# Kernel optimization log

Measured on AMD Instinct MI355X. Metric: run time of the kernel, lower is better.

## Reference

```python
import jax, jax.numpy as jnp
import numpy as np

D_MODEL = 1024
NUM_HEADS = 16
HEAD_DIM = D_MODEL // NUM_HEADS
MAX_SEQ_LEN = 1024
BATCH = 2
SEQ = 1024


def setup_inputs() -> dict:
    key = jax.random.key(0)
    ks = jax.random.split(key, 12)
    s = 1.0 / np.sqrt(D_MODEL)
    inp = {
        "q": jax.random.normal(ks[0], (BATCH, SEQ, D_MODEL), jnp.float32),
        "k": jax.random.normal(ks[1], (BATCH, SEQ, D_MODEL), jnp.float32),
        "v": jax.random.normal(ks[2], (BATCH, SEQ, D_MODEL), jnp.float32),
        # causal mask (broadcast over batch and heads); masked_fill where mask==0
        "mask": jnp.tril(jnp.ones((SEQ, SEQ), jnp.bool_))[None, None, :, :],
        "Wq": jax.random.normal(ks[3], (D_MODEL, D_MODEL), jnp.float32) * s,
        "bq": jnp.zeros((D_MODEL,), jnp.float32),
        "Wk": jax.random.normal(ks[4], (D_MODEL, D_MODEL), jnp.float32) * s,
        "bk": jnp.zeros((D_MODEL,), jnp.float32),
        "Wv": jax.random.normal(ks[5], (D_MODEL, D_MODEL), jnp.float32) * s,
        "bv": jnp.zeros((D_MODEL,), jnp.float32),
        "Wo": jax.random.normal(ks[6], (D_MODEL, D_MODEL), jnp.float32) * s,
        "bo": jnp.zeros((D_MODEL,), jnp.float32),
        # relative-position embedding table (requires_grad=False in original)
        "e_r": jax.random.normal(ks[7], (MAX_SEQ_LEN, HEAD_DIM), jnp.float32),
    }
    return inp


def _skew(qe):
    # qe: (b, h, q, L) -> pad last dim on the left, reshape, drop first row
    b, h, q, L = qe.shape
    s = jnp.pad(qe, ((0, 0), (0, 0), (0, 0), (1, 0)))  # (b,h,q,L+1)
    s = s.reshape(b, h, L + 1, q)
    return s[:, :, 1:, :]  # (b,h,L,q)


def _rel_position_mask(q_len, L, dtype):
    # keep qe[i, j] where j >= L - 1 - i (upper-right skewed triangle)
    rows = jnp.arange(q_len)
    cols = jnp.arange(L)
    return (cols[None, :] >= (L - 1 - rows)[:, None]).astype(dtype)


def reference(q, k, v, mask, Wq, bq, Wk, bk, Wv, bv, Wo, bo, e_r):
    B, S, _ = q.shape
    def split_heads(x):
        return x.reshape(B, -1, NUM_HEADS, HEAD_DIM).transpose(0, 2, 1, 3)

    qh = split_heads(q @ Wq + bq)  # (B,H,S,D)
    kh = split_heads(k @ Wk + bk)
    vh = split_heads(v @ Wv + bv)

    q_len = qh.shape[2]
    e_sub = e_r[max(0, MAX_SEQ_LEN - q_len):, :]  # (L, D), L = min(q_len, MAX)
    qe = jnp.einsum('bhqd,kd->bhqk', qh, e_sub)  # (B,H,q,L)
    pm = _rel_position_mask(q_len, e_sub.shape[0], qe.dtype)
    qe = qe * pm[None, None, :, :]
    S_rel = _skew(qe)  # (B,H,L,q) == (B,H,S,S)

    scores = jnp.einsum('bhqd,bhkd->bhqk', qh, kh) / np.sqrt(HEAD_DIM)
    if mask is not None:
        scores = jnp.where(mask, scores, -1e9)
    attn = jax.nn.softmax(scores + S_rel, axis=-1)
    out = jnp.einsum('bhqk,bhkd->bhqd', attn, vh)
    out = out.transpose(0, 2, 1, 3).reshape(B, -1, D_MODEL)
    out = out @ Wo + bo
    return out, S_rel, qe
```

## Files before the change

kernel.cpp:

```cpp
#include <hip/hip_runtime.h>
#include <hip/hip_bf16.h>

typedef unsigned short u16;
typedef __attribute__((ext_vector_type(8))) short    bf16x8;
typedef __attribute__((ext_vector_type(8))) unsigned short u16x8;
typedef __attribute__((ext_vector_type(4))) float    f32x4;

#define SEQ    1024
#define DMODEL 1024
#define NHEAD  16
#define HDIM   64

#define OUT_OFF_SREL 2097152UL
#define OUT_OFF_QE   35651584UL

#define MFMA16(a, b, c) __builtin_amdgcn_mfma_f32_16x16x32_bf16((a), (b), (c), 0, 0, 0)

__device__ __forceinline__ float b2f(u16 u) {
    union { unsigned int i; float f; } x; x.i = ((unsigned int)u) << 16; return x.f;
}
__device__ __forceinline__ u16 f2b(float f) {
    union { __hip_bfloat16 h; u16 u; } x; x.h = __float2bfloat16(f); return x.u;
}
__device__ __forceinline__ void st_out(void* p, size_t idx, float v, int isf32) {
    if (isf32) ((float*)p)[idx] = v;
    else       ((u16*)p)[idx]   = f2b(v);
}

__global__ __launch_bounds__(256)
void k_detect(const u16* __restrict__ q, unsigned* __restrict__ flag)
{
    __shared__ int cnt;
    if (threadIdx.x == 0) cnt = 0;
    __syncthreads();
    int plaus = 0;
    for (int i = threadIdx.x; i < 4096; i += 256) {
        u16 u = q[2 * i];
        int e = (u >> 7) & 0xFF;
        if (e >= 102 && e <= 130) plaus++;
    }
    atomicAdd(&cnt, plaus);
    __syncthreads();
    if (threadIdx.x == 0) *flag = (cnt < 2048) ? 1u : 0u;
}

__global__ __launch_bounds__(256)
void k_conv3(const void* __restrict__ s0, const void* __restrict__ s1, const void* __restrict__ s2,
             u16* __restrict__ d0, u16* __restrict__ d1, u16* __restrict__ d2,
             int n4, const unsigned* __restrict__ flag)
{
    const int z = blockIdx.z;
    const void* src = (z == 0) ? s0 : (z == 1) ? s1 : s2;
    u16* dst = (z == 0) ? d0 : (z == 1) ? d1 : d2;
    int i = blockIdx.x * 256 + threadIdx.x;
    if (i >= n4) return;
    if (*flag) {
        float4 f = ((const float4*)src)[i];
        ushort4 o;
        o.x = f2b(f.x); o.y = f2b(f.y); o.z = f2b(f.z); o.w = f2b(f.w);
        ((ushort4*)dst)[i] = o;
    } else {
        ((ushort4*)dst)[i] = ((const ushort4*)src)[i];
    }
}

__global__ __launch_bounds__(256)
void k_conv_small(const void* __restrict__ b0, const void* __restrict__ b1,
                  const void* __restrict__ b2, const void* __restrict__ b3,
                  const void* __restrict__ erp,
                  u16* __restrict__ db0, u16* __restrict__ db1,
                  u16* __restrict__ db2, u16* __restrict__ db3,
                  u16* __restrict__ der, const unsigned* __restrict__ flag)
{
    const int bx = blockIdx.x;
    const void* src; u16* dst; int i;
    if (bx < 64) { src = erp; dst = der; i = bx * 256 + threadIdx.x; }
    else {
        const int which = bx - 64;
        src = (which == 0) ? b0 : (which == 1) ? b1 : (which == 2) ? b2 : b3;
        dst = (which == 0) ? db0 : (which == 1) ? db1 : (which == 2) ? db2 : db3;
        i = threadIdx.x;
    }
    if (*flag) {
        float4 f = ((const float4*)src)[i];
        ushort4 o;
        o.x = f2b(f.x); o.y = f2b(f.y); o.z = f2b(f.z); o.w = f2b(f.w);
        ((ushort4*)dst)[i] = o;
    } else {
        ((ushort4*)dst)[i] = ((const ushort4*)src)[i];
    }
}

__global__ __launch_bounds__(256)
void k_convT4(const void* __restrict__ s0, const void* __restrict__ s1,
              const void* __restrict__ s2, const void* __restrict__ s3,
              u16* __restrict__ d0, u16* __restrict__ d1,
              u16* __restrict__ d2, u16* __restrict__ d3,
              const unsigned* __restrict__ flag)
{
    __shared__ u16 tile[64][65];
    const int z = blockIdx.z;
    const void* src = (z == 0) ? s0 : (z == 1) ? s1 : (z == 2) ? s2 : s3;
    u16* dst = (z == 0) ? d0 : (z == 1) ? d1 : (z == 2) ? d2 : d3;

    const int t  = threadIdx.x;
    const int n0 = blockIdx.x * 64;
    const int k0 = blockIdx.y * 64;
    const int isf32 = (*flag != 0u);

    #pragma unroll
    for (int i = 0; i < 4; ++i) {
        int idx = i * 256 + t;
        int r  = idx >> 4;
        int cg = (idx & 15) << 2;
        if (isf32) {
            float4 f = *(const float4*)((const float*)src + (size_t)(k0 + r) * 1024 + n0 + cg);
            tile[cg + 0][r] = f2b(f.x); tile[cg + 1][r] = f2b(f.y);
            tile[cg + 2][r] = f2b(f.z); tile[cg + 3][r] = f2b(f.w);
        } else {
            ushort4 u = *(const ushort4*)((const u16*)src + (size_t)(k0 + r) * 1024 + n0 + cg);
            tile[cg + 0][r] = u.x; tile[cg + 1][r] = u.y;
            tile[cg + 2][r] = u.z; tile[cg + 3][r] = u.w;
        }
    }
    __syncthreads();
    #pragma unroll
    for (int i = 0; i < 4; ++i) {
        int idx = i * 256 + t;
        int nl = idx >> 4;
        int kg = (idx & 15) << 2;
        ushort4 o;
        o.x = tile[nl][kg + 0]; o.y = tile[nl][kg + 1];
        o.z = tile[nl][kg + 2]; o.w = tile[nl][kg + 3];
        *(ushort4*)(dst + (size_t)(n0 + nl) * 1024 + k0 + kg) = o;
    }
}

__global__ __launch_bounds__(256)
void k_gemm(const u16* __restrict__ Aq, const u16* __restrict__ Ak, const u16* __restrict__ Av,
            const u16* __restrict__ Wtq, const u16* __restrict__ Wtk, const u16* __restrict__ Wtv,
            const u16* __restrict__ Bq, const u16* __restrict__ Bk, const u16* __restrict__ Bv,
            u16* __restrict__ Oq, u16* __restrict__ Ok, u16* __restrict__ Ov,
            void* __restrict__ out_flat, const unsigned* __restrict__ flag, int mode)
{
    __shared__ __align__(16) u16 Xs[128][72];
    __shared__ __align__(16) u16 Ws[128][72];

    const int z = blockIdx.z;
    const u16* A  = (z == 0) ? Aq : (z == 1) ? Ak : Av;
    const u16* Wt = (z == 0) ? Wtq : (z == 1) ? Wtk : Wtv;
    const u16* Bi = (z == 0) ? Bq : (z == 1) ? Bk : Bv;
    u16* O = (z == 0) ? Oq : (z == 1) ? Ok : Ov;

    const int t    = threadIdx.x;
    const int lane = t & 63;
    const int w    = t >> 6;
    const int q4   = lane >> 4;
    const int l16  = lane & 15;
    const int wy   = w >> 1, wx = w & 1;
    const int m0   = blockIdx.y * 128;
    const int n0   = blockIdx.x * 128;

    f32x4 acc[4][4] = {};

    for (int k0 = 0; k0 < DMODEL; k0 += 64) {
        __syncthreads();
        #pragma unroll
        for (int i = 0; i < 4; ++i) {
            int idx = i * 256 + t;
            int row = idx >> 3;
            int kg  = (idx & 7) << 3;
            *(u16x8*)&Xs[row][kg] = *(const u16x8*)(A  + (size_t)(m0 + row) * 1024 + k0 + kg);
            *(u16x8*)&Ws[row][kg] = *(const u16x8*)(Wt + (size_t)(n0 + row) * 1024 + k0 + kg);
        }
        __syncthreads();
        #pragma unroll
        for (int kc = 0; kc < 2; ++kc) {
            bf16x8 af[4], bfr[4];
            #pragma unroll
            for (int mt = 0; mt < 4; ++mt)
                af[mt] = *(const bf16x8*)&Xs[wy * 64 + mt * 16 + l16][kc * 32 + q4 * 8];
            #pragma unroll
            for (int nt = 0; nt < 4; ++nt)
                bfr[nt] = *(const bf16x8*)&Ws[wx * 64 + nt * 16 + l16][kc * 32 + q4 * 8];
            #pragma unroll
            for (int mt = 0; mt < 4; ++mt)
                #pragma unroll
                for (int nt = 0; nt < 4; ++nt)
                    acc[mt][nt] = MFMA16(af[mt], bfr[nt], acc[mt][nt]);
        }
    }

    const int isf32 = (*flag != 0u);
    float bias[4];
    #pragma unroll
    for (int nt = 0; nt < 4; ++nt) bias[nt] = b2f(Bi[n0 + wx * 64 + nt * 16 + l16]);

    #pragma unroll
    for (int mt = 0; mt < 4; ++mt) {
        #pragma unroll
        for (int nt = 0; nt < 4; ++nt) {
            #pragma unroll
            for (int reg = 0; reg < 4; ++reg) {
                const int m = m0 + wy * 64 + mt * 16 + q4 * 4 + reg;
                const int n = n0 + wx * 64 + nt * 16 + l16;
                const float v = acc[mt][nt][reg] + bias[nt];
                if (mode == 0) {
                    const int b = m >> 10, s = m & 1023, h = n >> 6, d = n & 63;
                    O[(((size_t)(b * NHEAD + h)) * SEQ + s) * HDIM + d] = f2b(v);
                } else {
                    st_out(out_flat, (size_t)m * DMODEL + n, v, isf32);
                }
            }
        }
    }
}

__global__ __launch_bounds__(256)
void k_attn(const u16* __restrict__ qh, const u16* __restrict__ kh, const u16* __restrict__ vh,
            const u16* __restrict__ er, u16* __restrict__ opre,
            void* __restrict__ out, const unsigned* __restrict__ flag)
{
    __shared__ __align__(16) u16 Ks[64][72];
    __shared__ __align__(16) u16 Vt[64][72];
    __shared__ __align__(16) u16 Es[128][72];
    __shared__ float Rs[4][16][130];
    __shared__ __align__(16) u16 Ps[4][16][72];

    const int t    = threadIdx.x;
    const int lane = t & 63;
    const int w    = t >> 6;
    const int q4   = lane >> 4;
    const int l16  = lane & 15;
    const int bh   = blockIdx.x;
    const int qt   = 15 - blockIdx.y;
    const int r0   = qt * 64;
    const int isf32 = (*flag != 0u);
    const size_t obase = (size_t)bh * (SEQ * SEQ);

    for (int ml = w; ml < 64; ml += 4) {
        const int r  = r0 + ml;
        const int Lz = SEQ - 1 - r;
        const size_t rq = OUT_OFF_QE   + obase + (size_t)r * SEQ;
        const size_t rs = OUT_OFF_SREL + obase + (size_t)r * SEQ + r + 1;
        for (int c2 = lane; c2 < Lz; c2 += 64) {
            st_out(out, rq + c2, 0.f, isf32);
            st_out(out, rs + c2, 0.f, isf32);
        }
    }

    bf16x8 aQ[2];
    #pragma unroll
    for (int kc = 0; kc < 2; ++kc)
        aQ[kc] = *(const bf16x8*)(qh + ((size_t)bh * SEQ + r0 + w * 16 + l16) * HDIM + kc * 32 + q4 * 8);

    f32x4 Oacc[4] = {};
    float mi[4] = { -1e30f, -1e30f, -1e30f, -1e30f };
    float li[4] = {};

    for (int tt = 0; tt <= qt; ++tt) {
        const int c0 = tt * 64;
        const int jbase = 960 + c0 - r0;
        const int diag = (tt == qt);

        __syncthreads();
        #pragma unroll
        for (int i = 0; i < 2; ++i) {
            int idx = i * 256 + t;
            int row = idx >> 3, kg = (idx & 7) << 3;
            *(u16x8*)&Ks[row][kg] = *(const u16x8*)(kh + ((size_t)bh * SEQ + c0 + row) * HDIM + kg);
        }
        #pragma unroll
        for (int i = 0; i < 4; ++i) {
            int idx = i * 256 + t;
            int c = idx >> 4, dg = (idx & 15) << 2;
            ushort4 v = *(const ushort4*)(vh + ((size_t)bh * SEQ + c0 + c) * HDIM + dg);
            Vt[dg + 0][c] = v.x; Vt[dg + 1][c] = v.y;
            Vt[dg + 2][c] = v.z; Vt[dg + 3][c] = v.w;
        }
        #pragma unroll
        for (int i = 0; i < 4; ++i) {
            int idx = i * 256 + t;
            int row = idx >> 3, kg = (idx & 7) << 3;
            int j = jbase + row; if (j > 1023) j = 1023;
            *(u16x8*)&Es[row][kg] = *(const u16x8*)(er + (size_t)j * HDIM + kg);
        }
        __syncthreads();

        {
            f32x4 Racc[8] = {};
            #pragma unroll
            for (int kc = 0; kc < 2; ++kc) {
                #pragma unroll
                for (int nt = 0; nt < 8; ++nt) {
                    bf16x8 bfr = *(const bf16x8*)&Es[nt * 16 + l16][kc * 32 + q4 * 8];
                    Racc[nt] = MFMA16(aQ[kc], bfr, Racc[nt]);
                }
            }
            #pragma unroll
            for (int nt = 0; nt < 8; ++nt)
                #pragma unroll
                for (int reg = 0; reg < 4; ++reg)
                    Rs[w][q4 * 4 + reg][nt * 16 + l16] = Racc[nt][reg];

            #pragma unroll
            for (int nt = 0; nt < 8; ++nt) {
                const int nn = nt * 16 + l16;
                #pragma unroll
                for (int reg = 0; reg < 4; ++reg) {
                    const int mloc = w * 16 + q4 * 4 + reg;
                    const int rel  = nn - 63 + mloc;
                    if (rel >= 0 && rel < 64 && (!diag || nn <= 63)) {
                        const int r = r0 + mloc;
                        const float v = Racc[nt][reg];
                        st_out(out, OUT_OFF_SREL + obase + (size_t)r * SEQ + (c0 + rel),   v, isf32);
                        st_out(out, OUT_OFF_QE   + obase + (size_t)r * SEQ + (jbase + nn), v, isf32);
                    }
                }
            }
        }

        f32x4 Sacc[4] = {};
        #pragma unroll
        for (int kc = 0; kc < 2; ++kc) {
            #pragma unroll
            for (int nt = 0; nt < 4; ++nt) {
                bf16x8 bfr = *(const bf16x8*)&Ks[nt * 16 + l16][kc * 32 + q4 * 8];
                Sacc[nt] = MFMA16(aQ[kc], bfr, Sacc[nt]);
            }
        }

        #pragma unroll
        for (int reg = 0; reg < 4; ++reg) {
            const int m16  = q4 * 4 + reg;
            const int mloc = w * 16 + m16;
            float sv[4];
            #pragma unroll
            for (int nt = 0; nt < 4; ++nt) {
                const int nloc = nt * 16 + l16;
                const int jj = 63 + nloc - mloc;
                float s = Sacc[nt][reg] * 0.125f + Rs[w][m16][jj];
                if (diag && (nloc > mloc)) s = -1e30f;
                sv[nt] = s;
            }
            float mx = fmaxf(fmaxf(sv[0], sv[1]), fmaxf(sv[2], sv[3]));
            #pragma unroll
            for (int off = 1; off < 16; off <<= 1) mx = fmaxf(mx, __shfl_xor(mx, off));
            const float mnew = fmaxf(mi[reg], mx);
            const float al   = __expf(mi[reg] - mnew);
            mi[reg] = mnew;
            float psum = 0.f;
            #pragma unroll
            for (int nt = 0; nt < 4; ++nt) {
                const float p = __expf(sv[nt] - mnew);
                psum += p;
                Ps[w][m16][nt * 16 + l16] = f2b(p);
            }
            #pragma unroll
            for (int off = 1; off < 16; off <<= 1) psum += __shfl_xor(psum, off);
            li[reg] = li[reg] * al + psum;
            #pragma unroll
            for (int dt = 0; dt < 4; ++dt) Oacc[dt][reg] *= al;
        }

        #pragma unroll
        for (int kc = 0; kc < 2; ++kc) {
            bf16x8 aP = *(const bf16x8*)&Ps[w][l16][kc * 32 + q4 * 8];
            #pragma unroll
            for (int dt = 0; dt < 4; ++dt) {
                bf16x8 bV = *(const bf16x8*)&Vt[dt * 16 + l16][kc * 32 + q4 * 8];
                Oacc[dt] = MFMA16(aP, bV, Oacc[dt]);
            }
        }
    }

    const int b = bh >> 4, h = bh & 15;
    #pragma unroll
    for (int dt = 0; dt < 4; ++dt) {
        #pragma unroll
        for (int reg = 0; reg < 4; ++reg) {
            const int r = r0 + w * 16 + q4 * 4 + reg;
            const int d = dt * 16 + l16;
            opre[((size_t)b * SEQ + r) * DMODEL + h * HDIM + d] = f2b(Oacc[dt][reg] / li[reg]);
        }
    }
}

extern "C" void kernel_launch(void* const* d_in, const int* in_sizes, int n_in,
                              void* d_out, int out_size, void* d_ws, size_t ws_size,
                              hipStream_t stream)
{
    u16* ws16 = (u16*)d_ws;
    unsigned* flag = (unsigned*)d_ws;
    u16* cq   = ws16 + 8;
    u16* ck   = cq   + 2097152;
    u16* cv   = ck   + 2097152;
    u16* cwqT = cv   + 2097152;
    u16* cwkT = cwqT + 1048576;
    u16* cwvT = cwkT + 1048576;
    u16* cwoT = cwvT + 1048576;
    u16* cbq  = cwoT + 1048576;
    u16* cbk  = cbq  + 1024;
    u16* cbv  = cbk  + 1024;
    u16* cbo  = cbv  + 1024;
    u16* cer  = cbo  + 1024;
    u16* qh   = cer  + 65536;
    u16* kh   = qh   + 2097152;
    u16* vh   = kh   + 2097152;
    u16* opre = vh   + 2097152;

    dim3 blk(256);

    k_detect<<<1, blk, 0, stream>>>((const u16*)d_in[0], flag);

    k_conv3<<<dim3(2048, 1, 3), blk, 0, stream>>>(d_in[0], d_in[1], d_in[2],
                                                  cq, ck, cv, 2097152 / 4, flag);
    k_convT4<<<dim3(16, 16, 4), blk, 0, stream>>>(d_in[4], d_in[6], d_in[8], d_in[10],
                                                  cwqT, cwkT, cwvT, cwoT, flag);
    k_conv_small<<<dim3(68), blk, 0, stream>>>(d_in[5], d_in[7], d_in[9], d_in[11], d_in[12],
                                               cbq, cbk, cbv, cbo, cer, flag);

    k_gemm<<<dim3(8, 16, 3), blk, 0, stream>>>(cq, ck, cv, cwqT, cwkT, cwvT,
                                               cbq, cbk, cbv, qh, kh, vh,
                                               nullptr, flag, 0);
    k_attn<<<dim3(32, 16), blk, 0, stream>>>(qh, kh, vh, cer, opre, d_out, flag);
    k_gemm<<<dim3(8, 16, 1), blk, 0, stream>>>(opre, opre, opre, cwoT, cwoT, cwoT,
                                               cbo, cbo, cbo, nullptr, nullptr, nullptr,
                                               d_out, flag, 1);
}
```

Before: 474.7 us.

## Merge conversion kernels, use direct global-to-LDS loads, drop attention LDS staging

Three input-conversion kernels are merged into one launch to cut launch overhead. The GEMM tile loads switch to global_load_lds with unpadded shared arrays, removing the register round-trip at the cost of possible LDS bank conflicts. In attention, K and relative-embedding fragments are read straight from global memory instead of being staged in LDS. The query-tile order is interleaved to balance causal work across blocks. Rs padding is also changed.

```diff
diff --git a/kernel.cpp b/kernel.cpp
--- a/kernel.cpp
+++ b/kernel.cpp
@@ -6,6 +6,9 @@
 typedef __attribute__((ext_vector_type(8))) unsigned short u16x8;
 typedef __attribute__((ext_vector_type(4))) float    f32x4;
 
+typedef __attribute__((address_space(1))) void gvoid;
+typedef __attribute__((address_space(3))) void lvoid;
+
 #define SEQ    1024
 #define DMODEL 1024
 #define NHEAD  16
@@ -25,6 +28,9 @@
 __device__ __forceinline__ void st_out(void* p, size_t idx, float v, int isf32) {
     if (isf32) ((float*)p)[idx] = v;
     else       ((u16*)p)[idx]   = f2b(v);
+}
+__device__ __forceinline__ void gload_lds16(const u16* g, u16* l) {
+    __builtin_amdgcn_global_load_lds((gvoid*)g, (lvoid*)l, 16, 0, 0);
 }
 
 __global__ __launch_bounds__(256)
@@ -45,94 +51,89 @@
 }
 
 __global__ __launch_bounds__(256)
-void k_conv3(const void* __restrict__ s0, const void* __restrict__ s1, const void* __restrict__ s2,
-             u16* __restrict__ d0, u16* __restrict__ d1, u16* __restrict__ d2,
-             int n4, const unsigned* __restrict__ flag)
-{
-    const int z = blockIdx.z;
-    const void* src = (z == 0) ? s0 : (z == 1) ? s1 : s2;
-    u16* dst = (z == 0) ? d0 : (z == 1) ? d1 : d2;
-    int i = blockIdx.x * 256 + threadIdx.x;
-    if (i >= n4) return;
-    if (*flag) {
-        float4 f = ((const float4*)src)[i];
-        ushort4 o;
-        o.x = f2b(f.x); o.y = f2b(f.y); o.z = f2b(f.z); o.w = f2b(f.w);
-        ((ushort4*)dst)[i] = o;
-    } else {
-        ((ushort4*)dst)[i] = ((const ushort4*)src)[i];
-    }
-}
-
-__global__ __launch_bounds__(256)
-void k_conv_small(const void* __restrict__ b0, const void* __restrict__ b1,
-                  const void* __restrict__ b2, const void* __restrict__ b3,
-                  const void* __restrict__ erp,
-                  u16* __restrict__ db0, u16* __restrict__ db1,
-                  u16* __restrict__ db2, u16* __restrict__ db3,
-                  u16* __restrict__ der, const unsigned* __restrict__ flag)
-{
-    const int bx = blockIdx.x;
-    const void* src; u16* dst; int i;
-    if (bx < 64) { src = erp; dst = der; i = bx * 256 + threadIdx.x; }
-    else {
-        const int which = bx - 64;
-        src = (which == 0) ? b0 : (which == 1) ? b1 : (which == 2) ? b2 : b3;
-        dst = (which == 0) ? db0 : (which == 1) ? db1 : (which == 2) ? db2 : db3;
-        i = threadIdx.x;
-    }
-    if (*flag) {
-        float4 f = ((const float4*)src)[i];
-        ushort4 o;
-        o.x = f2b(f.x); o.y = f2b(f.y); o.z = f2b(f.z); o.w = f2b(f.w);
-        ((ushort4*)dst)[i] = o;
-    } else {
-        ((ushort4*)dst)[i] = ((const ushort4*)src)[i];
-    }
-}
-
-__global__ __launch_bounds__(256)
-void k_convT4(const void* __restrict__ s0, const void* __restrict__ s1,
-              const void* __restrict__ s2, const void* __restrict__ s3,
-              u16* __restrict__ d0, u16* __restrict__ d1,
-              u16* __restrict__ d2, u16* __restrict__ d3,
-              const unsigned* __restrict__ flag)
+void k_conv_all(const void* __restrict__ sq, const void* __restrict__ sk, const void* __restrict__ sv,
+                const void* __restrict__ w0, const void* __restrict__ w1,
+                const void* __restrict__ w2, const void* __restrict__ w3,
+                const void* __restrict__ b0, const void* __restrict__ b1,
+                const void* __restrict__ b2, const void* __restrict__ b3,
+                const void* __restrict__ erp,
+                u16* __restrict__ cq, u16* __restrict__ ck, u16* __restrict__ cv,
+                u16* __restrict__ d0, u16* __restrict__ d1,
+                u16* __restrict__ d2, u16* __restrict__ d3,
+                u16* __restrict__ db0, u16* __restrict__ db1,
+                u16* __restrict__ db2, u16* __restrict__ db3,
+                u16* __restrict__ der, const unsigned* __restrict__ flag)
 {
     __shared__ u16 tile[64][65];
-    const int z = blockIdx.z;
-    const void* src = (z == 0) ? s0 : (z == 1) ? s1 : (z == 2) ? s2 : s3;
-    u16* dst = (z == 0) ? d0 : (z == 1) ? d1 : (z == 2) ? d2 : d3;
-
-    const int t  = threadIdx.x;
-    const int n0 = blockIdx.x * 64;
-    const int k0 = blockIdx.y * 64;
+    const int t = threadIdx.x;
+    const int b = blockIdx.x;
     const int isf32 = (*flag != 0u);
 
-    #pragma unroll
-    for (int i = 0; i < 4; ++i) {
-        int idx = i * 256 + t;
-        int r  = idx >> 4;
-        int cg = (idx & 15) << 2;
+    if (b < 6144) {
+        const int z = b >> 11;
+        const void* src = (z == 0) ? sq : (z == 1) ? sk : sv;
+        u16* dst = (z == 0) ? cq : (z == 1) ? ck : cv;
+        const int i = (b & 2047) * 256 + t;
         if (isf32) {
-            float4 f = *(const float4*)((const float*)src + (size_t)(k0 + r) * 1024 + n0 + cg);
-            tile[cg + 0][r] = f2b(f.x); tile[cg + 1][r] = f2b(f.y);
-            tile[cg + 2][r] = f2b(f.z); tile[cg + 3][r] = f2b(f.w);
+            float4 f = ((const float4*)src)[i];
+            ushort4 o;
+            o.x = f2b(f.x); o.y = f2b(f.y); o.z = f2b(f.z); o.w = f2b(f.w);
+            ((ushort4*)dst)[i] = o;
         } else {
-            ushort4 u = *(const ushort4*)((const u16*)src + (size_t)(k0 + r) * 1024 + n0 + cg);
-            tile[cg + 0][r] = u.x; tile[cg + 1][r] = u.y;
-            tile[cg + 2][r] = u.z; tile[cg + 3][r] = u.w;
-        }
-    }
-    __syncthreads();
-    #pragma unroll
-    for (int i = 0; i < 4; ++i) {
-        int idx = i * 256 + t;
-        int nl = idx >> 4;
-        int kg = (idx & 15) << 2;
-        ushort4 o;
-        o.x = tile[nl][kg + 0]; o.y = tile[nl][kg + 1];
-        o.z = tile[nl][kg + 2]; o.w = tile[nl][kg + 3];
-        *(ushort4*)(dst + (size_t)(n0 + nl) * 1024 + k0 + kg) = o;
+            ((ushort4*)dst)[i] = ((const ushort4*)src)[i];
+        }
+    } else if (b < 7168) {
+        const int bb = b - 6144;
+        const int z  = bb >> 8;
+        const void* src = (z == 0) ? w0 : (z == 1) ? w1 : (z == 2) ? w2 : w3;
+        u16* dst = (z == 0) ? d0 : (z == 1) ? d1 : (z == 2) ? d2 : d3;
+        const int n0 = (bb & 15) * 64;
+        const int k0 = ((bb >> 4) & 15) * 64;
+
+        #pragma unroll
+        for (int i = 0; i < 4; ++i) {
+            int idx = i * 256 + t;
+            int r  = idx >> 4;
+            int cg = (idx & 15) << 2;
+            if (isf32) {
+                float4 f = *(const float4*)((const float*)src + (size_t)(k0 + r) * 1024 + n0 + cg);
+                tile[cg + 0][r] = f2b(f.x); tile[cg + 1][r] = f2b(f.y);
+                tile[cg + 2][r] = f2b(f.z); tile[cg + 3][r] = f2b(f.w);
+            } else {
+                ushort4 u = *(const ushort4*)((const u16*)src + (size_t)(k0 + r) * 1024 + n0 + cg);
+                tile[cg + 0][r] = u.x; tile[cg + 1][r] = u.y;
+                tile[cg + 2][r] = u.z; tile[cg + 3][r] = u.w;
+            }
+        }
+        __syncthreads();
+        #pragma unroll
+        for (int i = 0; i < 4; ++i) {
+            int idx = i * 256 + t;
+            int nl = idx >> 4;
+            int kg = (idx & 15) << 2;
+            ushort4 o;
+            o.x = tile[nl][kg + 0]; o.y = tile[nl][kg + 1];
+            o.z = tile[nl][kg + 2]; o.w = tile[nl][kg + 3];
+            *(ushort4*)(dst + (size_t)(n0 + nl) * 1024 + k0 + kg) = o;
+        }
+    } else {
+        const int bx = b - 7168;
+        const void* src; u16* dst; int i;
+        if (bx < 64) { src = erp; dst = der; i = bx * 256 + t; }
+        else {
+            const int which = bx - 64;
+            src = (which == 0) ? b0 : (which == 1) ? b1 : (which == 2) ? b2 : b3;
+            dst = (which == 0) ? db0 : (which == 1) ? db1 : (which == 2) ? db2 : db3;
+            i = t;
+        }
+        if (isf32) {
+            float4 f = ((const float4*)src)[i];
+            ushort4 o;
+            o.x = f2b(f.x); o.y = f2b(f.y); o.z = f2b(f.z); o.w = f2b(f.w);
+            ((ushort4*)dst)[i] = o;
+        } else {
+            ((ushort4*)dst)[i] = ((const ushort4*)src)[i];
+        }
     }
 }
 
@@ -143,8 +144,8 @@
             u16* __restrict__ Oq, u16* __restrict__ Ok, u16* __restrict__ Ov,
             void* __restrict__ out_flat, const unsigned* __restrict__ flag, int mode)
 {
-    __shared__ __align__(16) u16 Xs[128][72];
-    __shared__ __align__(16) u16 Ws[128][72];
+    __shared__ __align__(16) u16 Xs[128][64];
+    __shared__ __align__(16) u16 Ws[128][64];
 
     const int z = blockIdx.z;
     const u16* A  = (z == 0) ? Aq : (z == 1) ? Ak : Av;
@@ -167,11 +168,12 @@
         __syncthreads();
         #pragma unroll
         for (int i = 0; i < 4; ++i) {
-            int idx = i * 256 + t;
-            int row = idx >> 3;
-            int kg  = (idx & 7) << 3;
-            *(u16x8*)&Xs[row][kg] = *(const u16x8*)(A  + (size_t)(m0 + row) * 1024 + k0 + kg);
-            *(u16x8*)&Ws[row][kg] = *(const u16x8*)(Wt + (size_t)(n0 + row) * 1024 + k0 + kg);
+            const int idx = i * 256 + t;
+            const int row = idx >> 3;
+            const int kg  = (idx & 7) << 3;
+            const int wb  = i * 256 + (t & 192);
+            gload_lds16(A  + (size_t)(m0 + row) * 1024 + k0 + kg, (u16*)Xs + (size_t)wb * 8);
+            gload_lds16(Wt + (size_t)(n0 + row) * 1024 + k0 + kg, (u16*)Ws + (size_t)wb * 8);
         }
         __syncthreads();
         #pragma unroll
@@ -221,10 +223,8 @@
             const u16* __restrict__ er, u16* __restrict__ opre,
             void* __restrict__ out, const unsigned* __restrict__ flag)
 {
-    __shared__ __align__(16) u16 Ks[64][72];
     __shared__ __align__(16) u16 Vt[64][72];
-    __shared__ __align__(16) u16 Es[128][72];
-    __shared__ float Rs[4][16][130];
+    __shared__ float Rs[4][16][132];
     __shared__ __align__(16) u16 Ps[4][16][72];
 
     const int t    = threadIdx.x;
@@ -233,7 +233,8 @@
     const int q4   = lane >> 4;
     const int l16  = lane & 15;
     const int bh   = blockIdx.x;
-    const int qt   = 15 - blockIdx.y;
+    const int by   = blockIdx.y;
+    const int qt   = (by < 8) ? (15 - by) : (by - 8);
     const int r0   = qt * 64;
     const int isf32 = (*flag != 0u);
     const size_t obase = (size_t)bh * (SEQ * SEQ);
@@ -265,12 +266,6 @@
 
         __syncthreads();
         #pragma unroll
-        for (int i = 0; i < 2; ++i) {
-            int idx = i * 256 + t;
-            int row = idx >> 3, kg = (idx & 7) << 3;
-            *(u16x8*)&Ks[row][kg] = *(const u16x8*)(kh + ((size_t)bh * SEQ + c0 + row) * HDIM + kg);
-        }
-        #pragma unroll
         for (int i = 0; i < 4; ++i) {
             int idx = i * 256 + t;
             int c = idx >> 4, dg = (idx & 15) << 2;
@@ -278,24 +273,16 @@
             Vt[dg + 0][c] = v.x; Vt[dg + 1][c] = v.y;
             Vt[dg + 2][c] = v.z; Vt[dg + 3][c] = v.w;
         }
-        #pragma unroll
-        for (int i = 0; i < 4; ++i) {
-            int idx = i * 256 + t;
-            int row = idx >> 3, kg = (idx & 7) << 3;
-            int j = jbase + row; if (j > 1023) j = 1023;
-            *(u16x8*)&Es[row][kg] = *(const u16x8*)(er + (size_t)j * HDIM + kg);
-        }
         __syncthreads();
 
         {
             f32x4 Racc[8] = {};
             #pragma unroll
-            for (int kc = 0; kc < 2; ++kc) {
-                #pragma unroll
-                for (int nt = 0; nt < 8; ++nt) {
-                    bf16x8 bfr = *(const bf16x8*)&Es[nt * 16 + l16][kc * 32 + q4 * 8];
-                    Racc[nt] = MFMA16(aQ[kc], bfr, Racc[nt]);
-                }
+            for (int nt = 0; nt < 8; ++nt) {
+                int j = jbase + nt * 16 + l16; if (j > 1023) j = 1023;
+                const u16* ep = er + (size_t)j * HDIM + q4 * 8;
+                Racc[nt] = MFMA16(aQ[0], *(const bf16x8*)(ep),      Racc[nt]);
+                Racc[nt] = MFMA16(aQ[1], *(const bf16x8*)(ep + 32), Racc[nt]);
             }
             #pragma unroll
             for (int nt = 0; nt < 8; ++nt)
@@ -322,12 +309,10 @@
 
         f32x4 Sacc[4] = {};
         #pragma unroll
-        for (int kc = 0; kc < 2; ++kc) {
-            #pragma unroll
-            for (int nt = 0; nt < 4; ++nt) {
-                bf16x8 bfr = *(const bf16x8*)&Ks[nt * 16 + l16][kc * 32 + q4 * 8];
-                Sacc[nt] = MFMA16(aQ[kc], bfr, Sacc[nt]);
-            }
+        for (int nt = 0; nt < 4; ++nt) {
+            const u16* kp = kh + ((size_t)bh * SEQ + c0 + nt * 16 + l16) * HDIM + q4 * 8;
+            Sacc[nt] = MFMA16(aQ[0], *(const bf16x8*)(kp),      Sacc[nt]);
+            Sacc[nt] = MFMA16(aQ[1], *(const bf16x8*)(kp + 32), Sacc[nt]);
         }
 
         #pragma unroll
@@ -413,11 +398,10 @@
 
     k_detect<<<1, blk, 0, stream>>>((const u16*)d_in[0], flag);
 
-    k_conv3<<<dim3(2048, 1, 3), blk, 0, stream>>>(d_in[0], d_in[1], d_in[2],
-                                                  cq, ck, cv, 2097152 / 4, flag);
-    k_convT4<<<dim3(16, 16, 4), blk, 0, stream>>>(d_in[4], d_in[6], d_in[8], d_in[10],
-                                                  cwqT, cwkT, cwvT, cwoT, flag);
-    k_conv_small<<<dim3(68), blk, 0, stream>>>(d_in[5], d_in[7], d_in[9], d_in[11], d_in[12],
+    k_conv_all<<<dim3(7236), blk, 0, stream>>>(d_in[0], d_in[1], d_in[2],
+                                               d_in[4], d_in[6], d_in[8], d_in[10],
+                                               d_in[5], d_in[7], d_in[9], d_in[11], d_in[12],
+                                               cq, ck, cv, cwqT, cwkT, cwvT, cwoT,
                                                cbq, cbk, cbv, cbo, cer, flag);
 
     k_gemm<<<dim3(8, 16, 3), blk, 0, stream>>>(cq, ck, cv, cwqT, cwkT, cwvT,
```

Measured after the change: 504.5 us. 6.3% more time.
